# Optimization experiments

Hardware: AMD Instinct MI355X
Metric: run time of the kernel (lower is better)

Reference implementation:

```python
import jax, jax.numpy as jnp
import numpy as np

N_HEAD = 16
ROPE_THETA = 10000.0


def _rope_cache(T, dim, theta=ROPE_THETA):
    # inv_freq over even indices, as in RotaryEmbedding
    inv_freq = 1.0 / (theta ** (jnp.arange(0, dim, 2, dtype=jnp.float32) / dim))
    freqs = jnp.arange(T, dtype=jnp.float32)[:, None] * inv_freq[None, :]  # [T, dim//2]
    return jnp.cos(freqs), jnp.sin(freqs)


def _apply_rope(x, cos, sin):
    # x: [B, H, T, D]; cos/sin: [T, D//2] broadcast over B,H
    x1 = x[..., ::2]
    x2 = x[..., 1::2]
    # even slots: x1*cos - x2*sin ; odd slots: x2*cos + x1*sin (interleaved rotate-pairs)
    r1 = x1 * cos - x2 * sin
    r2 = x2 * cos + x1 * sin
    return jnp.stack([r1, r2], axis=-1).reshape(x.shape)


def setup_inputs() -> dict:
    key = jax.random.key(0)
    k1, k2, k3 = jax.random.split(key, 3)
    B, T, C = 4, 2048, 1024
    x = jax.random.normal(k1, (B, T, C), dtype=jnp.float32)
    W_qkv = jax.random.normal(k2, (C, 3 * C), dtype=jnp.float32) * (C ** -0.5)
    W_out = jax.random.normal(k3, (C, C), dtype=jnp.float32) * (C ** -0.5)
    return {"x": x, "W_qkv": W_qkv, "W_out": W_out}


def reference(x, W_qkv, W_out):
    B, T, C = x.shape
    H = N_HEAD
    D = C // H
    # fused QKV projection -> [3, B, H, T, D]
    qkv = (x @ W_qkv).reshape(B, T, 3, H, D).transpose(2, 0, 3, 1, 4)
    q, k, v = qkv[0], qkv[1], qkv[2]
    cos, sin = _rope_cache(T, D)
    q = _apply_rope(q, cos, sin)
    k = _apply_rope(k, cos, sin)
    scale = 1.0 / jnp.sqrt(jnp.float32(D))
    scores = jnp.einsum('bhqd,bhkd->bhqk', q, k) * scale  # [B,H,T,T]
    causal_mask = jnp.tril(jnp.ones((T, T), dtype=bool))
    scores = jnp.where(causal_mask, scores, -jnp.inf)
    attn = jax.nn.softmax(scores, axis=-1)
    out = jnp.einsum('bhqk,bhkd->bhqd', attn, v)  # [B,H,T,D]
    out = out.transpose(0, 2, 1, 3).reshape(B, T, C)
    return out @ W_out
```

## Files before the change

kernel.cpp:

```cpp
#include <hip/hip_runtime.h>
#include <hip/hip_bf16.h>
#include <math.h>

#define BATCH 4
#define SEQ   2048
#define CDIM  1024
#define NHEAD 16
#define HDIM  64
#define QKVN  3072
#define QSCALE 0.1803368801111244f

typedef float f32x4 __attribute__((ext_vector_type(4)));
typedef float f32x16 __attribute__((ext_vector_type(16)));
typedef short bf16x8 __attribute__((ext_vector_type(8)));
typedef short bf16x4 __attribute__((ext_vector_type(4)));
typedef int i32x2 __attribute__((ext_vector_type(2)));
typedef int i32x4 __attribute__((ext_vector_type(4)));

static __device__ __forceinline__ unsigned short f2bf(float f) {
    unsigned int u = __float_as_uint(f);
    u += 0x7FFF + ((u >> 16) & 1);
    return (unsigned short)(u >> 16);
}
static __device__ __forceinline__ float bf2f(unsigned short u) {
    return __uint_as_float(((unsigned int)u) << 16);
}
static __device__ __forceinline__ unsigned int pk2bf(float lo, float hi) {
    __hip_bfloat162 h = __float22bfloat162_rn(make_float2(lo, hi));
    return *(unsigned int*)&h;
}
static __device__ __forceinline__ bf16x8 lds_read8(const unsigned short* p) {
    bf16x4 lo = *(const bf16x4*)p;
    bf16x4 hi = *(const bf16x4*)(p + 4);
    return __builtin_shufflevector(lo, hi, 0, 1, 2, 3, 4, 5, 6, 7);
}

__global__ __launch_bounds__(256) void convert_bf16(const float* __restrict__ src,
                                                    unsigned short* __restrict__ dst,
                                                    int n4) {
    int i = blockIdx.x * 256 + threadIdx.x;
    if (i >= n4) return;
    float4 v = ((const float4*)src)[i];
    ushort4 o;
    o.x = f2bf(v.x); o.y = f2bf(v.y); o.z = f2bf(v.z); o.w = f2bf(v.w);
    ((ushort4*)dst)[i] = o;
}

__global__ __launch_bounds__(256) void transpose_bf16(const float* __restrict__ W,
                                                      unsigned short* __restrict__ Wt,
                                                      int K, int N) {
    __shared__ unsigned short tile[64][65];
    const int tid = threadIdx.x;
    const int n0 = blockIdx.x * 64;
    const int k0 = blockIdx.y * 64;
    const int r = tid >> 4;
    const int c4 = (tid & 15) << 2;
    #pragma unroll
    for (int ii = 0; ii < 4; ii++) {
        int row = r + 16 * ii;
        float4 v = *(const float4*)&W[(size_t)(k0 + row) * N + n0 + c4];
        tile[c4 + 0][row] = f2bf(v.x);
        tile[c4 + 1][row] = f2bf(v.y);
        tile[c4 + 2][row] = f2bf(v.z);
        tile[c4 + 3][row] = f2bf(v.w);
    }
    __syncthreads();
    #pragma unroll
    for (int ii = 0; ii < 4; ii++) {
        int row = r + 16 * ii;
        ushort4 o;
        o.x = tile[row][c4 + 0];
        o.y = tile[row][c4 + 1];
        o.z = tile[row][c4 + 2];
        o.w = tile[row][c4 + 3];
        *(ushort4*)&Wt[(size_t)(n0 + row) * K + k0 + c4] = o;
    }
}

#define GLDS(gp, lp) __builtin_amdgcn_global_load_lds(                       \
    (const __attribute__((address_space(1))) unsigned int*)(gp),             \
    (__attribute__((address_space(3))) unsigned int*)(lp), 16, 0, 0)

template <typename OUT>
__global__ __launch_bounds__(256) void gemm_bt_bf16(
    const unsigned short* __restrict__ A,
    const unsigned short* __restrict__ Bt,
    OUT* __restrict__ C, int M, int N, int K) {
    __shared__ unsigned short As[128 * 32];
    __shared__ unsigned short Bs[128 * 32];

    const int tid = threadIdx.x;
    const int wave = tid >> 6;
    const int lane = tid & 63;
    const int bm = blockIdx.y * 128;
    const int bn = blockIdx.x * 128;
    const int wm = (wave >> 1) * 64;
    const int wn = (wave & 1) * 64;

    const int srow = tid >> 2;
    const int scol = (((tid & 3) ^ ((tid >> 3) & 3)) << 3);
    const unsigned short* Ag0 = A + (size_t)(bm + srow) * K + scol;
    const unsigned short* Ag1 = A + (size_t)(bm + 64 + srow) * K + scol;
    const unsigned short* Bg0 = Bt + (size_t)(bn + srow) * K + scol;
    const unsigned short* Bg1 = Bt + (size_t)(bn + 64 + srow) * K + scol;
    char* AsW = (char*)As + wave * 1024;
    char* BsW = (char*)Bs + wave * 1024;

    const int fm = lane & 15;
    const int quad = lane >> 4;
    const int ck = (quad ^ ((fm >> 1) & 3)) << 3;

    f32x4 acc[4][4];
    #pragma unroll
    for (int i = 0; i < 4; i++)
        #pragma unroll
        for (int j = 0; j < 4; j++)
            acc[i][j] = (f32x4){0.f, 0.f, 0.f, 0.f};

    for (int k0 = 0; k0 < K; k0 += 32) {
        GLDS(Ag0 + k0, AsW);
        GLDS(Ag1 + k0, AsW + 4096);
        GLDS(Bg0 + k0, BsW);
        GLDS(Bg1 + k0, BsW + 4096);
        __syncthreads();

        bf16x8 af[4], bfr[4];
        #pragma unroll
        for (int i = 0; i < 4; i++)
            af[i] = *(const bf16x8*)&As[(wm + i * 16 + fm) * 32 + ck];
        #pragma unroll
        for (int j = 0; j < 4; j++)
            bfr[j] = *(const bf16x8*)&Bs[(wn + j * 16 + fm) * 32 + ck];
        #pragma unroll
        for (int i = 0; i < 4; i++)
            #pragma unroll
            for (int j = 0; j < 4; j++)
                acc[i][j] = __builtin_amdgcn_mfma_f32_16x16x32_bf16(
                    af[i], bfr[j], acc[i][j], 0, 0, 0);
        __syncthreads();
    }

    const int er = quad * 4;
    #pragma unroll
    for (int i = 0; i < 4; i++) {
        #pragma unroll
        for (int j = 0; j < 4; j++) {
            #pragma unroll
            for (int r = 0; r < 4; r++) {
                size_t off = (size_t)(bm + wm + i * 16 + er + r) * N + bn + wn + j * 16 + fm;
                if constexpr (sizeof(OUT) == 2)
                    C[off] = f2bf(acc[i][j][r]);
                else
                    C[off] = acc[i][j][r];
            }
        }
    }
}

__global__ __launch_bounds__(256) void rope_qk(const unsigned short* __restrict__ qkvb,
                                               unsigned short* __restrict__ Qg,
                                               unsigned short* __restrict__ Kg) {
    const int i = blockIdx.x * 256 + threadIdx.x;
    const int c4 = (i & 15) << 2;
    const int h = (i >> 4) & 15;
    const int s = (i >> 8) & 1;
    const int t = (i >> 9) & 2047;
    const int b = i >> 20;

    ushort4 v = *(const ushort4*)&qkvb[(((size_t)(b * SEQ + t) * 3 + s) * CDIM) + h * HDIM + c4];
    float x0 = bf2f(v.x), x1 = bf2f(v.y), x2 = bf2f(v.z), x3 = bf2f(v.w);
    const float invf0 = powf(10000.0f, -((float)c4) / 64.0f);
    const float invf1 = powf(10000.0f, -((float)(c4 + 2)) / 64.0f);
    float s0, c0, s1, c1;
    __sincosf((float)t * invf0, &s0, &c0);
    __sincosf((float)t * invf1, &s1, &c1);
    const float sc = s == 0 ? QSCALE : 1.0f;
    ushort4 o;
    o.x = f2bf((x0 * c0 - x1 * s0) * sc);
    o.y = f2bf((x1 * c0 + x0 * s0) * sc);
    o.z = f2bf((x2 * c1 - x3 * s1) * sc);
    o.w = f2bf((x3 * c1 + x2 * s1) * sc);
    unsigned short* dst = (s == 0) ? Qg : Kg;
    *(ushort4*)&dst[((size_t)(b * NHEAD + h) * SEQ + t) * HDIM + c4] = o;
}

__global__ __launch_bounds__(256) void transpose_v(const unsigned short* __restrict__ qkvb,
                                                   unsigned short* __restrict__ Vtg) {
    __shared__ unsigned short tile[64 * 68];
    const int tid = threadIdx.x;
    const int tt = blockIdx.x;
    const int bh = blockIdx.y;
    const int b = bh >> 4, h = bh & 15;
    const int r = tid >> 4;
    const int c4 = (tid & 15) << 2;
    #pragma unroll
    for (int ii = 0; ii < 4; ii++) {
        int row = r + 16 * ii;
        ushort4 v = *(const ushort4*)&qkvb[(((size_t)(b * SEQ + tt * 64 + row) * 3 + 2) * CDIM) + h * HDIM + c4];
        *(ushort4*)&tile[row * 68 + c4] = v;
    }
    __syncthreads();
    #pragma unroll
    for (int ii = 0; ii < 4; ii++) {
        int d = r + 16 * ii;
        ushort4 o;
        o.x = tile[(c4 + 0) * 68 + d];
        o.y = tile[(c4 + 1) * 68 + d];
        o.z = tile[(c4 + 2) * 68 + d];
        o.w = tile[(c4 + 3) * 68 + d];
        *(ushort4*)&Vtg[((size_t)bh * HDIM + d) * SEQ + tt * 64 + c4] = o;
    }
}

__global__ __launch_bounds__(256, 4) void flash_attn_mfma(
    const unsigned short* __restrict__ Qg,
    const unsigned short* __restrict__ Kg,
    const unsigned short* __restrict__ Vtg,
    unsigned short* __restrict__ att) {
    __shared__ unsigned short Ks[2][64 * 68];
    __shared__ unsigned short Vt[2][64 * 68];

    const int tid = threadIdx.x;
    const int wave = tid >> 6;
    const int lane = tid & 63;
    const int l31 = lane & 31;
    const int hi = lane >> 5;
    const int wq = wave * 32;
    const int bh = blockIdx.x & 63;
    const int qt = 15 - (blockIdx.x >> 6);
    const int b = bh >> 4, h = bh & 15;

    const int r_ld = tid >> 4;
    const int c4 = (tid & 15) << 2;

    const unsigned short* Kbase = Kg + (size_t)bh * SEQ * HDIM;
    const unsigned short* Vbase = Vtg + (size_t)bh * HDIM * SEQ;

    const int qrow = qt * 128 + wq + l31;

    bf16x8 bq[4];
    #pragma unroll
    for (int dc = 0; dc < 4; dc++)
        bq[dc] = *(const bf16x8*)&Qg[((size_t)bh * SEQ + qrow) * HDIM + dc * 16 + hi * 8];

    f32x16 O[2];
    #pragma unroll
    for (int nt = 0; nt < 2; nt++)
        #pragma unroll
        for (int r = 0; r < 16; r++) O[nt][r] = 0.f;
    float lsum = 0.f;

    const int jtop = 2 * qt + 1;

    ushort4 kreg[4], vreg[4];
    #pragma unroll
    for (int ii = 0; ii < 4; ii++) {
        const int row = r_ld + 16 * ii;
        kreg[ii] = *(const ushort4*)&Kbase[(size_t)row * HDIM + c4];
        vreg[ii] = *(const ushort4*)&Vbase[(size_t)row * SEQ + c4];
    }
    #pragma unroll
    for (int ii = 0; ii < 4; ii++) {
        const int row = r_ld + 16 * ii;
        *(ushort4*)&Ks[0][row * 68 + c4] = kreg[ii];
        *(ushort4*)&Vt[0][row * 68 + c4] = vreg[ii];
    }
    __syncthreads();

    int cur = 0;
    #pragma unroll 1
    for (int j = 0; j <= jtop; j++) {
        if (j < jtop) {
            #pragma unroll
            for (int ii = 0; ii < 4; ii++) {
                const int row = r_ld + 16 * ii;
                kreg[ii] = *(const ushort4*)&Kbase[(size_t)((j + 1) * 64 + row) * HDIM + c4];
                vreg[ii] = *(const ushort4*)&Vbase[(size_t)row * SEQ + (j + 1) * 64 + c4];
            }
        }

        const bool active = (j * 64) <= (qt * 128 + wq + 31);
        if (active) {
            const unsigned short* Kc = Ks[cur];
            const unsigned short* Vc = Vt[cur];
            const bool diag = (j * 64 + 63) > (qt * 128 + wq);

            #pragma unroll
            for (int kt = 0; kt < 2; kt++) {
                f32x16 sa;
                #pragma unroll
                for (int r = 0; r < 16; r++) sa[r] = 0.f;
                __builtin_amdgcn_s_setprio(1);
                #pragma unroll
                for (int dc = 0; dc < 4; dc++) {
                    bf16x8 ak = lds_read8(&Kc[(kt * 32 + l31) * 68 + dc * 16 + hi * 8]);
                    sa = __builtin_amdgcn_mfma_f32_32x32x16_bf16(ak, bq[dc], sa, 0, 0, 0);
                }
                __builtin_amdgcn_s_setprio(0);

                if (diag) {
                    const int kb = j * 64 + kt * 32 + 4 * hi;
                    #pragma unroll
                    for (int r = 0; r < 16; r++) {
                        const int kg = kb + (r & 3) + 8 * (r >> 2);
                        if (kg > qrow) sa[r] = -INFINITY;
                    }
                }

                float e[16];
                #pragma unroll
                for (int r = 0; r < 16; r++) {
                    e[r] = exp2f(sa[r]);
                    lsum += e[r];
                }
                unsigned int p32[8];
                #pragma unroll
                for (int v = 0; v < 8; v++)
                    p32[v] = pk2bf(e[2 * v], e[2 * v + 1]);

                #pragma unroll
                for (int c = 0; c < 2; c++) {
                    i32x2 s0 = __builtin_amdgcn_permlane32_swap(
                        (int)p32[4 * c + 0], (int)p32[4 * c + 2], false, false);
                    i32x2 s1 = __builtin_amdgcn_permlane32_swap(
                        (int)p32[4 * c + 1], (int)p32[4 * c + 3], false, false);
                    i32x4 pw = (i32x4){s0[0], s1[0], s0[1], s1[1]};
                    bf16x8 pa = *(bf16x8*)&pw;
                    __builtin_amdgcn_s_setprio(1);
                    #pragma unroll
                    for (int nt = 0; nt < 2; nt++) {
                        bf16x8 bv = lds_read8(&Vc[(nt * 32 + l31) * 68 + kt * 32 + c * 16 + hi * 8]);
                        O[nt] = __builtin_amdgcn_mfma_f32_32x32x16_bf16(pa, bv, O[nt], 0, 0, 0);
                    }
                    __builtin_amdgcn_s_setprio(0);
                }
            }
        }

        if (j < jtop) {
            const int nb = cur ^ 1;
            #pragma unroll
            for (int ii = 0; ii < 4; ii++) {
                const int row = r_ld + 16 * ii;
                *(ushort4*)&Ks[nb][row * 68 + c4] = kreg[ii];
                *(ushort4*)&Vt[nb][row * 68 + c4] = vreg[ii];
            }
        }

        __syncthreads();
        cur ^= 1;
    }

    const float lfull = lsum + __shfl_xor(lsum, 32);
    const float inv = 1.0f / lfull;
    #pragma unroll
    for (int r = 0; r < 16; r++) {
        const int qloc = (r & 3) + 8 * (r >> 2) + 4 * hi;
        const float invr = __uint_as_float((unsigned int)__builtin_amdgcn_ds_bpermute(
            qloc * 4, (int)__float_as_uint(inv)));
        const int row = qt * 128 + wq + qloc;
        #pragma unroll
        for (int nt = 0; nt < 2; nt++)
            att[(size_t)(b * SEQ + row) * CDIM + h * HDIM + nt * 32 + l31] =
                f2bf(O[nt][r] * invr);
    }
}

extern "C" void kernel_launch(void* const* d_in, const int* in_sizes, int n_in,
                              void* d_out, int out_size, void* d_ws, size_t ws_size,
                              hipStream_t stream) {
    const float* x     = (const float*)d_in[0];
    const float* W_qkv = (const float*)d_in[1];
    const float* W_out = (const float*)d_in[2];
    float* out = (float*)d_out;

    const int M = BATCH * SEQ;

    unsigned short* qkvb = (unsigned short*)d_ws;
    unsigned short* xb   = qkvb + (size_t)M * QKVN;
    unsigned short* wqb  = xb + (size_t)M * CDIM;
    unsigned short* wob  = wqb + (size_t)CDIM * QKVN;
    unsigned short* attb = wob + (size_t)CDIM * CDIM;
    unsigned short* Qg   = attb + (size_t)M * CDIM;
    unsigned short* Kg   = Qg + (size_t)M * CDIM;
    unsigned short* Vtg  = Kg + (size_t)M * CDIM;

    convert_bf16<<<(M * CDIM / 4 + 255) / 256, 256, 0, stream>>>(x, xb, M * CDIM / 4);
    transpose_bf16<<<dim3(QKVN / 64, CDIM / 64), 256, 0, stream>>>(W_qkv, wqb, CDIM, QKVN);
    transpose_bf16<<<dim3(CDIM / 64, CDIM / 64), 256, 0, stream>>>(W_out, wob, CDIM, CDIM);

    gemm_bt_bf16<unsigned short><<<dim3(QKVN / 128, M / 128), 256, 0, stream>>>(
        xb, wqb, qkvb, M, QKVN, CDIM);

    rope_qk<<<(BATCH * SEQ * 2 * NHEAD * 16) / 256, 256, 0, stream>>>(qkvb, Qg, Kg);
    transpose_v<<<dim3(SEQ / 64, BATCH * NHEAD), 256, 0, stream>>>(qkvb, Vtg);

    flash_attn_mfma<<<BATCH * NHEAD * (SEQ / 128), 256, 0, stream>>>(Qg, Kg, Vtg, attb);

    gemm_bt_bf16<float><<<dim3(CDIM / 128, M / 128), 256, 0, stream>>>(
        attb, wob, out, M, CDIM, CDIM);
}
```

Before: 310.0 us.

## Fuse RoPE and V transpose into QKV GEMM epilogue with precomputed cos/sin table

The QKV projection GEMM now applies RoPE and the query scale, and writes Q/K in head-major layout plus a transposed V directly from its epilogue. Tiles are staged through LDS in two passes. This removes the intermediate qkv buffer round trip and two separate kernels. A small kernel precomputes a cos/sin table so the epilogue avoids powf and sincos per element. The cost is extra LDS staging, barriers and strided global stores in the GEMM epilogue.

```diff
diff --git a/kernel.cpp b/kernel.cpp
--- a/kernel.cpp
+++ b/kernel.cpp
@@ -33,6 +33,16 @@
     bf16x4 lo = *(const bf16x4*)p;
     bf16x4 hi = *(const bf16x4*)(p + 4);
     return __builtin_shufflevector(lo, hi, 0, 1, 2, 3, 4, 5, 6, 7);
+}
+
+__global__ __launch_bounds__(256) void build_ctab(float2* __restrict__ ctab) {
+    const int i = blockIdx.x * 256 + threadIdx.x;
+    const int dp = i & 31;
+    const int t = i >> 5;
+    const float invf = powf(10000.0f, -((float)(2 * dp)) / 64.0f);
+    float sv, cv;
+    __sincosf((float)t * invf, &sv, &cv);
+    ctab[i] = make_float2(cv, sv);
 }
 
 __global__ __launch_bounds__(256) void convert_bf16(const float* __restrict__ src,
@@ -157,58 +167,126 @@
     }
 }
 
-__global__ __launch_bounds__(256) void rope_qk(const unsigned short* __restrict__ qkvb,
-                                               unsigned short* __restrict__ Qg,
-                                               unsigned short* __restrict__ Kg) {
-    const int i = blockIdx.x * 256 + threadIdx.x;
-    const int c4 = (i & 15) << 2;
-    const int h = (i >> 4) & 15;
-    const int s = (i >> 8) & 1;
-    const int t = (i >> 9) & 2047;
-    const int b = i >> 20;
-
-    ushort4 v = *(const ushort4*)&qkvb[(((size_t)(b * SEQ + t) * 3 + s) * CDIM) + h * HDIM + c4];
-    float x0 = bf2f(v.x), x1 = bf2f(v.y), x2 = bf2f(v.z), x3 = bf2f(v.w);
-    const float invf0 = powf(10000.0f, -((float)c4) / 64.0f);
-    const float invf1 = powf(10000.0f, -((float)(c4 + 2)) / 64.0f);
-    float s0, c0, s1, c1;
-    __sincosf((float)t * invf0, &s0, &c0);
-    __sincosf((float)t * invf1, &s1, &c1);
-    const float sc = s == 0 ? QSCALE : 1.0f;
-    ushort4 o;
-    o.x = f2bf((x0 * c0 - x1 * s0) * sc);
-    o.y = f2bf((x1 * c0 + x0 * s0) * sc);
-    o.z = f2bf((x2 * c1 - x3 * s1) * sc);
-    o.w = f2bf((x3 * c1 + x2 * s1) * sc);
-    unsigned short* dst = (s == 0) ? Qg : Kg;
-    *(ushort4*)&dst[((size_t)(b * NHEAD + h) * SEQ + t) * HDIM + c4] = o;
-}
-
-__global__ __launch_bounds__(256) void transpose_v(const unsigned short* __restrict__ qkvb,
-                                                   unsigned short* __restrict__ Vtg) {
-    __shared__ unsigned short tile[64 * 68];
+__global__ __launch_bounds__(256) void gemm_qkv_fused(
+    const unsigned short* __restrict__ A,
+    const unsigned short* __restrict__ Bt,
+    const float2* __restrict__ ctab,
+    unsigned short* __restrict__ Qg,
+    unsigned short* __restrict__ Kg,
+    unsigned short* __restrict__ Vtg) {
+    __shared__ unsigned short SH[8448];
+    unsigned short* As = SH;
+    unsigned short* Bs = SH + 4096;
+    const int K = CDIM;
+
     const int tid = threadIdx.x;
-    const int tt = blockIdx.x;
-    const int bh = blockIdx.y;
-    const int b = bh >> 4, h = bh & 15;
-    const int r = tid >> 4;
-    const int c4 = (tid & 15) << 2;
-    #pragma unroll
-    for (int ii = 0; ii < 4; ii++) {
-        int row = r + 16 * ii;
-        ushort4 v = *(const ushort4*)&qkvb[(((size_t)(b * SEQ + tt * 64 + row) * 3 + 2) * CDIM) + h * HDIM + c4];
-        *(ushort4*)&tile[row * 68 + c4] = v;
-    }
-    __syncthreads();
-    #pragma unroll
-    for (int ii = 0; ii < 4; ii++) {
-        int d = r + 16 * ii;
-        ushort4 o;
-        o.x = tile[(c4 + 0) * 68 + d];
-        o.y = tile[(c4 + 1) * 68 + d];
-        o.z = tile[(c4 + 2) * 68 + d];
-        o.w = tile[(c4 + 3) * 68 + d];
-        *(ushort4*)&Vtg[((size_t)bh * HDIM + d) * SEQ + tt * 64 + c4] = o;
+    const int wave = tid >> 6;
+    const int lane = tid & 63;
+    const int bm = blockIdx.y * 128;
+    const int bn = blockIdx.x * 128;
+    const int wm = (wave >> 1) * 64;
+    const int wn = (wave & 1) * 64;
+
+    const int srow = tid >> 2;
+    const int scol = (((tid & 3) ^ ((tid >> 3) & 3)) << 3);
+    const unsigned short* Ag0 = A + (size_t)(bm + srow) * K + scol;
+    const unsigned short* Ag1 = A + (size_t)(bm + 64 + srow) * K + scol;
+    const unsigned short* Bg0 = Bt + (size_t)(bn + srow) * K + scol;
+    const unsigned short* Bg1 = Bt + (size_t)(bn + 64 + srow) * K + scol;
+    char* AsW = (char*)SH + wave * 1024;
+    char* BsW = (char*)SH + 8192 + wave * 1024;
+
+    const int fm = lane & 15;
+    const int quad = lane >> 4;
+    const int ck = (quad ^ ((fm >> 1) & 3)) << 3;
+
+    f32x4 acc[4][4];
+    #pragma unroll
+    for (int i = 0; i < 4; i++)
+        #pragma unroll
+        for (int j = 0; j < 4; j++)
+            acc[i][j] = (f32x4){0.f, 0.f, 0.f, 0.f};
+
+    for (int k0 = 0; k0 < K; k0 += 32) {
+        GLDS(Ag0 + k0, AsW);
+        GLDS(Ag1 + k0, AsW + 4096);
+        GLDS(Bg0 + k0, BsW);
+        GLDS(Bg1 + k0, BsW + 4096);
+        __syncthreads();
+
+        bf16x8 af[4], bfr[4];
+        #pragma unroll
+        for (int i = 0; i < 4; i++)
+            af[i] = *(const bf16x8*)&As[(wm + i * 16 + fm) * 32 + ck];
+        #pragma unroll
+        for (int j = 0; j < 4; j++)
+            bfr[j] = *(const bf16x8*)&Bs[(wn + j * 16 + fm) * 32 + ck];
+        #pragma unroll
+        for (int i = 0; i < 4; i++)
+            #pragma unroll
+            for (int j = 0; j < 4; j++)
+                acc[i][j] = __builtin_amdgcn_mfma_f32_16x16x32_bf16(
+                    af[i], bfr[j], acc[i][j], 0, 0, 0);
+        __syncthreads();
+    }
+
+    const int s = bn >> 10;
+    const int hbase = (bn & 1023) >> 6;
+    const int b = bm >> 11;
+    const int t0 = bm & 2047;
+
+    #pragma unroll 1
+    for (int pass = 0; pass < 2; pass++) {
+        if ((wave >> 1) == pass) {
+            #pragma unroll
+            for (int i = 0; i < 4; i++)
+                #pragma unroll
+                for (int j = 0; j < 4; j++)
+                    #pragma unroll
+                    for (int r = 0; r < 4; r++)
+                        SH[(i * 16 + quad * 4 + r) * 132 + wn + j * 16 + fm] =
+                            f2bf(acc[i][j][r]);
+        }
+        __syncthreads();
+
+        if (s < 2) {
+            unsigned short* dst = (s == 0) ? Qg : Kg;
+            const float sc = (s == 0) ? QSCALE : 1.0f;
+            #pragma unroll
+            for (int it = 0; it < 16; it++) {
+                const int idx = it * 256 + tid;
+                const int row = idx >> 6;
+                const int col = (idx & 63) << 1;
+                const unsigned int pr = *(const unsigned int*)&SH[row * 132 + col];
+                const float x0 = bf2f((unsigned short)pr);
+                const float x1 = bf2f((unsigned short)(pr >> 16));
+                const int t = t0 + pass * 64 + row;
+                const int h = hbase + (col >> 6);
+                const int d = col & 63;
+                const float2 cs = ctab[t * 32 + (d >> 1)];
+                const float r0 = (x0 * cs.x - x1 * cs.y) * sc;
+                const float r1 = (x1 * cs.x + x0 * cs.y) * sc;
+                *(unsigned int*)&dst[((size_t)(b * NHEAD + h) * SEQ + t) * HDIM + d] =
+                    pk2bf(r0, r1);
+            }
+        } else {
+            #pragma unroll
+            for (int it = 0; it < 8; it++) {
+                const int idx = it * 256 + tid;
+                const int dcol = idx >> 4;
+                const int tq = idx & 15;
+                ushort4 o;
+                o.x = SH[(tq * 4 + 0) * 132 + dcol];
+                o.y = SH[(tq * 4 + 1) * 132 + dcol];
+                o.z = SH[(tq * 4 + 2) * 132 + dcol];
+                o.w = SH[(tq * 4 + 3) * 132 + dcol];
+                const int h = hbase + (dcol >> 6);
+                const int dl = dcol & 63;
+                const int t = t0 + pass * 64 + tq * 4;
+                *(ushort4*)&Vtg[((size_t)(b * NHEAD + h) * HDIM + dl) * SEQ + t] = o;
+            }
+        }
+        __syncthreads();
     }
 }
 
@@ -376,8 +454,8 @@
 
     const int M = BATCH * SEQ;
 
-    unsigned short* qkvb = (unsigned short*)d_ws;
-    unsigned short* xb   = qkvb + (size_t)M * QKVN;
+    float2* ctab = (float2*)d_ws;
+    unsigned short* xb   = (unsigned short*)(ctab + SEQ * 32);
     unsigned short* wqb  = xb + (size_t)M * CDIM;
     unsigned short* wob  = wqb + (size_t)CDIM * QKVN;
     unsigned short* attb = wob + (size_t)CDIM * CDIM;
@@ -385,15 +463,13 @@
     unsigned short* Kg   = Qg + (size_t)M * CDIM;
     unsigned short* Vtg  = Kg + (size_t)M * CDIM;
 
+    build_ctab<<<(SEQ * 32) / 256, 256, 0, stream>>>(ctab);
     convert_bf16<<<(M * CDIM / 4 + 255) / 256, 256, 0, stream>>>(x, xb, M * CDIM / 4);
     transpose_bf16<<<dim3(QKVN / 64, CDIM / 64), 256, 0, stream>>>(W_qkv, wqb, CDIM, QKVN);
     transpose_bf16<<<dim3(CDIM / 64, CDIM / 64), 256, 0, stream>>>(W_out, wob, CDIM, CDIM);
 
-    gemm_bt_bf16<unsigned short><<<dim3(QKVN / 128, M / 128), 256, 0, stream>>>(
-        xb, wqb, qkvb, M, QKVN, CDIM);
-
-    rope_qk<<<(BATCH * SEQ * 2 * NHEAD * 16) / 256, 256, 0, stream>>>(qkvb, Qg, Kg);
-    transpose_v<<<dim3(SEQ / 64, BATCH * NHEAD), 256, 0, stream>>>(qkvb, Vtg);
+    gemm_qkv_fused<<<dim3(QKVN / 128, M / 128), 256, 0, stream>>>(
+        xb, wqb, ctab, Qg, Kg, Vtg);
 
     flash_attn_mfma<<<BATCH * NHEAD * (SEQ / 128), 256, 0, stream>>>(Qg, Kg, Vtg, attb);
 
```

Measured after the change: 270.6 us. 1.15x faster.
